# Kernel tuning notes

Measured on AMD Instinct MI355X. Metric: run time of the kernel, lower is better.

## Reference

```python
import jax, jax.numpy as jnp
import numpy as np

EPS = 1e-5
SLOPE = 0.01  # LeakyReLU negative_slope

def _ln(x, g, b):
    m = jnp.mean(x, axis=-1, keepdims=True)
    v = jnp.mean((x - m) ** 2, axis=-1, keepdims=True)
    return (x - m) * jax.lax.rsqrt(v + EPS) * g + b

def _lrelu(x):
    return jnp.where(x >= 0, x, SLOPE * x)

def _s6(x, W1, b1, W2, b2, W3, b3, A):
    # x: (B, L, D); A: (D, N). Mamba-style S6 selective scan.
    Bm = x @ W2 + b2                       # (B, L, N) input-dependent B
    Cm = x @ W3 + b3                       # (B, L, N) input-dependent C
    delta = jax.nn.softplus(x @ W1 + b1)   # (B, L, D) step sizes
    dA = jnp.exp(jnp.einsum('bld,dn->bldn', delta, A))            # (B,L,D,N)
    dBx = jnp.einsum('bld,bln->bldn', delta, Bm) * x[..., None]    # (B,L,D,N) dB * x
    Bsz, L, D = x.shape
    N = A.shape[1]
    def step(h, inp):
        dA_t, dBx_t, C_t = inp
        h = dA_t * h + dBx_t                       # (B, D, N)
        return h, jnp.einsum('bn,bdn->bd', C_t, h)  # y_t: (B, D)
    xs = (jnp.transpose(dA, (1, 0, 2, 3)),
          jnp.transpose(dBx, (1, 0, 2, 3)),
          jnp.transpose(Cm, (1, 0, 2)))
    _, ys = jax.lax.scan(step, jnp.zeros((Bsz, D, N), x.dtype), xs)
    return jnp.transpose(ys, (1, 0, 2))  # (B, L, D)

def _fwd(text, audio, video, tW1, tb1, tg1, tbe1, tW2, tb2, tg2, tbe2, sW1, sb1, sW2, sb2, sW3, sb3, sA, aW1, ab1, ag1, abe1, aW2, ab2, ag2, abe2, vW1, vb1, vg1, vbe1, vW2, vb2, vg2, vbe2, cW1, cb1, cW2, cb2):
    # text branch: Linear+LN+LeakyReLU x2, Dropout(eval=identity), S6
    t = _lrelu(_ln(text @ tW1 + tb1, tg1, tbe1))
    t = _lrelu(_ln(t @ tW2 + tb2, tg2, tbe2))
    t = _s6(t, sW1, sb1, sW2, sb2, sW3, sb3, sA)
    # audio / video branches are computed but do not feed the output (as in source)
    a = _lrelu(_ln(audio @ aW1 + ab1, ag1, abe1))
    a = _lrelu(_ln(a @ aW2 + ab2, ag2, abe2))
    v = _lrelu(_ln(video @ vW1 + vb1, vg1, vbe1))
    v = _lrelu(_ln(v @ vW2 + vb2, vg2, vbe2))
    o1 = t @ cW1 + cb1
    return o1 @ cW2 + cb2  # (B, L, 2)

def setup_inputs() -> dict:
    key = jax.random.key(0)
    ks = iter(jax.random.split(key, 64))
    def W(shape, s=0.05):
        return jax.random.normal(next(ks), shape, jnp.float32) * s
    B, L = 64, 63
    d = {
        'text': jax.random.normal(next(ks), (B, L, 100), jnp.float32),
        'audio': jax.random.normal(next(ks), (B, L, 73), jnp.float32),
        'video': jax.random.normal(next(ks), (B, L, 100), jnp.float32),
        'tW1': W((100, 128)), 'tb1': jnp.zeros(128), 'tg1': jnp.ones(128), 'tbe1': jnp.zeros(128),
        'tW2': W((128, 100)), 'tb2': jnp.zeros(100), 'tg2': jnp.ones(100), 'tbe2': jnp.zeros(100),
        'sW1': W((100, 100)), 'sb1': jnp.zeros(100),
        'sW2': W((100, 300)), 'sb2': jnp.zeros(300),
        'sW3': W((100, 300)), 'sb3': jnp.zeros(300),
        'sA': jnp.full((100, 300), 1.0 / np.sqrt(300.0), jnp.float32),  # F.normalize(ones, dim=-1)
        'aW1': W((73, 256)), 'ab1': jnp.zeros(256), 'ag1': jnp.ones(256), 'abe1': jnp.zeros(256),
        'aW2': W((256, 100)), 'ab2': jnp.zeros(100), 'ag2': jnp.ones(100), 'abe2': jnp.zeros(100),
        'vW1': W((100, 256)), 'vb1': jnp.zeros(256), 'vg1': jnp.ones(256), 'vbe1': jnp.zeros(256),
        'vW2': W((256, 100)), 'vb2': jnp.zeros(100), 'vg2': jnp.ones(100), 'vbe2': jnp.zeros(100),
        'cW1': W((100, 50)), 'cb1': jnp.zeros(50),
        'cW2': W((50, 2)), 'cb2': jnp.zeros(2),
    }
    return d

def reference(text, audio, video, tW1, tb1, tg1, tbe1, tW2, tb2, tg2, tbe2, sW1, sb1, sW2, sb2, sW3, sb3, sA, aW1, ab1, ag1, abe1, aW2, ab2, ag2, abe2, vW1, vb1, vg1, vbe1, vW2, vb2, vg2, vbe2, cW1, cb1, cW2, cb2):
    return _fwd(text, audio, video, tW1, tb1, tg1, tbe1, tW2, tb2, tg2, tbe2, sW1, sb1, sW2, sb2, sW3, sb3, sA, aW1, ab1, ag1, abe1, aW2, ab2, ag2, abe2, vW1, vb1, vg1, vbe1, vW2, vb2, vg2, vbe2, cW1, cb1, cW2, cb2)
```

## Files before the change

### kernel.cpp

```cpp
#include <hip/hip_runtime.h>
#include <hip/hip_bf16.h>


typedef __hip_bfloat16 bf16;

#define BATCH 64
#define SEQ   63
#define ROWS  (BATCH * SEQ)
#define DIN   100
#define H1    128
#define DM    100
#define NS    300

__device__ __forceinline__ float2 up2(unsigned u) {
    float2 r;
    r.x = __uint_as_float(u << 16);
    r.y = __uint_as_float(u & 0xffff0000u);
    return r;
}
template<bool ISB>
__device__ __forceinline__ float LD(const void* p, int i) {
    if (ISB) return __bfloat162float(((const bf16*)p)[i]);
    else     return ((const float*)p)[i];
}
template<bool ISB>
__device__ __forceinline__ float2 LD2(const void* p, int i) {
    if (ISB) return up2(((const unsigned*)p)[i]);
    else     return ((const float2*)p)[i];
}
__device__ __forceinline__ float waveReduceSum(float v) {
#pragma unroll
    for (int off = 32; off > 0; off >>= 1) v += __shfl_xor(v, off, 64);
    return v;
}
__device__ __forceinline__ float4 waveReduceSum4(float4 v) {
#pragma unroll
    for (int off = 32; off > 0; off >>= 1) {
        const float a = __shfl_xor(v.x, off, 64);
        const float b = __shfl_xor(v.y, off, 64);
        const float c = __shfl_xor(v.z, off, 64);
        const float d = __shfl_xor(v.w, off, 64);
        v.x += a; v.y += b; v.z += c; v.w += d;
    }
    return v;
}
__device__ __forceinline__ float lrelu(float x) { return x >= 0.f ? x : 0.01f * x; }
__device__ __forceinline__ float softplusf(float x) {
    return (x > 20.f) ? x : log1pf(__expf(x));
}
__device__ __forceinline__ bool flags_uniform(const float* __restrict__ f) {
    bool u = true;
#pragma unroll
    for (int i = 0; i < 8; ++i) u &= (f[i] > 0.5f);
    return u;
}
__device__ __forceinline__ bool detect_bf16(const unsigned short* __restrict__ probe) {
    const int l = threadIdx.x & 63;
    const unsigned u0 = probe[l * 2];
    const unsigned u1 = probe[l * 2 + 1];
    const float v0 = fabsf(__uint_as_float(u0 << 16));
    const float v1 = fabsf(__uint_as_float(u1 << 16));
    const bool big = !(v0 < 1000.f) || !(v1 < 1000.f);
    const bool zero_even = (u0 == 0u);
    const unsigned long long mb = __ballot(big);
    const unsigned long long mz = __ballot(zero_even);
    return (mb == 0ULL) && (__popcll(mz) < 32);
}

template<bool ISB>
__device__ __forceinline__ void a_main(
    const void* __restrict__ text,
    const void* __restrict__ tW1, const void* __restrict__ tb1,
    const void* __restrict__ tg1, const void* __restrict__ tbe1,
    const void* __restrict__ tW2, const void* __restrict__ tb2,
    const void* __restrict__ tg2, const void* __restrict__ tbe2,
    const void* __restrict__ sW1w, const void* __restrict__ sb1,
    float* __restrict__ ddx, float* __restrict__ t2g,
    float* __restrict__ sW,
    float (&xb)[4][DIN][2], float (&t1b)[4][H1][2], float (&t2b)[4][DM][2])
{
    const int tid  = threadIdx.x;
    const int w    = tid >> 6;
    const int lane = tid & 63;
    const int r0   = blockIdx.x * 8 + w * 2;

    if (lane < 50) {
#pragma unroll
        for (int r = 0; r < 2; ++r) {
            const float2 xv = LD2<ISB>(text, (r0 + r) * 50 + lane);
            xb[w][2 * lane][r]     = xv.x;
            xb[w][2 * lane + 1][r] = xv.y;
        }
    }
    for (int i = tid; i < 6400; i += 256)
        *(float2*)&sW[2 * i] = LD2<ISB>(tW1, i);
    __syncthreads();

    const float2 b1v = LD2<ISB>(tb1, lane);
    float ax0 = b1v.x, ay0 = b1v.y, ax1 = b1v.x, ay1 = b1v.y;
#pragma unroll 10
    for (int k = 0; k < DIN; ++k) {
        const float2 wv = *(const float2*)&sW[k * 128 + 2 * lane];
        const float2 xv = *(const float2*)&xb[w][k][0];
        ax0 += xv.x * wv.x; ay0 += xv.x * wv.y;
        ax1 += xv.y * wv.x; ay1 += xv.y * wv.y;
    }
    {
        float4 red = waveReduceSum4(make_float4(
            ax0 + ay0, ax0 * ax0 + ay0 * ay0,
            ax1 + ay1, ax1 * ax1 + ay1 * ay1));
        const float m0 = red.x * (1.f / 128.f);
        const float rs0 = rsqrtf(red.y * (1.f / 128.f) - m0 * m0 + 1e-5f);
        const float m1 = red.z * (1.f / 128.f);
        const float rs1 = rsqrtf(red.w * (1.f / 128.f) - m1 * m1 + 1e-5f);
        const float2 g = LD2<ISB>(tg1, lane), be = LD2<ISB>(tbe1, lane);
        float2 v;
        v.x = lrelu((ax0 - m0) * rs0 * g.x + be.x);
        v.y = lrelu((ax1 - m1) * rs1 * g.x + be.x);
        *(float2*)&t1b[w][2 * lane][0] = v;
        v.x = lrelu((ay0 - m0) * rs0 * g.y + be.y);
        v.y = lrelu((ay1 - m1) * rs1 * g.y + be.y);
        *(float2*)&t1b[w][2 * lane + 1][0] = v;
    }
    __syncthreads();

    for (int i = tid; i < 6400; i += 256)
        *(float2*)&sW[2 * i] = LD2<ISB>(tW2, i);
    __syncthreads();

    const bool act = lane < 50;
    const int  li  = act ? lane : 0;
    const float2 b2v = LD2<ISB>(tb2, li);
    float cx0 = b2v.x, cy0 = b2v.y, cx1 = b2v.x, cy1 = b2v.y;
#pragma unroll 8
    for (int k = 0; k < H1; ++k) {
        const float2 wv = *(const float2*)&sW[k * 100 + 2 * li];
        const float2 tv = *(const float2*)&t1b[w][k][0];
        cx0 += tv.x * wv.x; cy0 += tv.x * wv.y;
        cx1 += tv.y * wv.x; cy1 += tv.y * wv.y;
    }
    float u0x, u0y, u1x, u1y;
    {
        float4 red = waveReduceSum4(act ? make_float4(
            cx0 + cy0, cx0 * cx0 + cy0 * cy0,
            cx1 + cy1, cx1 * cx1 + cy1 * cy1) : make_float4(0.f, 0.f, 0.f, 0.f));
        const float m0 = red.x * 0.01f;
        const float rs0 = rsqrtf(red.y * 0.01f - m0 * m0 + 1e-5f);
        const float m1 = red.z * 0.01f;
        const float rs1 = rsqrtf(red.w * 0.01f - m1 * m1 + 1e-5f);
        if (act) {
            const float2 g = LD2<ISB>(tg2, lane), be = LD2<ISB>(tbe2, lane);
            u0x = lrelu((cx0 - m0) * rs0 * g.x + be.x);
            u0y = lrelu((cy0 - m0) * rs0 * g.y + be.y);
            u1x = lrelu((cx1 - m1) * rs1 * g.x + be.x);
            u1y = lrelu((cy1 - m1) * rs1 * g.y + be.y);
            t2b[w][2 * lane][0] = u0x; t2b[w][2 * lane + 1][0] = u0y;
            t2b[w][2 * lane][1] = u1x; t2b[w][2 * lane + 1][1] = u1y;
            *(float2*)(t2g + (r0)     * DM + 2 * lane) = make_float2(u0x, u0y);
            *(float2*)(t2g + (r0 + 1) * DM + 2 * lane) = make_float2(u1x, u1y);
        }
    }
    __syncthreads();

    for (int i = tid; i < 5000; i += 256)
        *(float2*)&sW[2 * i] = LD2<ISB>(sW1w, i);
    __syncthreads();

    const float2 sbv = LD2<ISB>(sb1, li);
    float dA0x = sbv.x, dA0y = sbv.y, dA1x = sbv.x, dA1y = sbv.y;
#pragma unroll 10
    for (int k = 0; k < DM; ++k) {
        const float2 wv = *(const float2*)&sW[k * 100 + 2 * li];
        const float2 tv = *(const float2*)&t2b[w][k][0];
        dA0x += tv.x * wv.x; dA0y += tv.x * wv.y;
        dA1x += tv.y * wv.x; dA1y += tv.y * wv.y;
    }
    if (act) {
        float de0 = softplusf(dA0x), de1 = softplusf(dA0y);
        float4 o;
        o.x = de0; o.y = de0 * u0x; o.z = de1; o.w = de1 * u0y;
        *(float4*)(ddx + (r0) * (2 * DM) + 4 * lane) = o;
        de0 = softplusf(dA1x); de1 = softplusf(dA1y);
        o.x = de0; o.y = de0 * u1x; o.z = de1; o.w = de1 * u1y;
        *(float4*)(ddx + (r0 + 1) * (2 * DM) + 4 * lane) = o;
    }
}

template<bool ISB>
__device__ __forceinline__ void a_prep(
    const void* __restrict__ sW2, const void* __restrict__ sb2,
    const void* __restrict__ sW3, const void* __restrict__ sb3,
    float* __restrict__ M33p, float* __restrict__ k0w, float* __restrict__ sW,
    int d3)
{
    const int tid = threadIdx.x;
    const int w = tid >> 6, lane = tid & 63;
    float* W3row = sW;
    float* b2v   = sW + 320;
    float* b3v   = sW + 640;
    for (int i = tid; i < 300; i += 256) {
        W3row[i] = LD<ISB>(sW3, d3 * 300 + i);
        b2v[i]   = LD<ISB>(sb2, i);
        b3v[i]   = LD<ISB>(sb3, i);
    }
    __syncthreads();
    for (int g = 0; g < 6; ++g) {
        const int d2 = w * 25 + g * 4;
        float4 p = make_float4(0.f, 0.f, 0.f, 0.f);
#pragma unroll
        for (int rep = 0; rep < 5; ++rep) {
            const int n = lane + 64 * rep;
            if (n < 300) {
                const float w3 = W3row[n];
                p.x += LD<ISB>(sW2, (d2 + 0) * 300 + n) * w3;
                p.y += LD<ISB>(sW2, (d2 + 1) * 300 + n) * w3;
                p.z += LD<ISB>(sW2, (d2 + 2) * 300 + n) * w3;
                p.w += LD<ISB>(sW2, (d2 + 3) * 300 + n) * w3;
            }
        }
        p = waveReduceSum4(p);
        if (lane == 0) {
            M33p[d3 * 102 + d2 + 0] = p.x;
            M33p[d3 * 102 + d2 + 1] = p.y;
            M33p[d3 * 102 + d2 + 2] = p.z;
            M33p[d3 * 102 + d2 + 3] = p.w;
        }
    }
    {
        const int d2 = w * 25 + 24;
        float4 p = make_float4(0.f, 0.f, 0.f, 0.f);
#pragma unroll
        for (int rep = 0; rep < 5; ++rep) {
            const int n = lane + 64 * rep;
            if (n < 300) {
                p.x += LD<ISB>(sW2, d2 * 300 + n) * W3row[n];
                if (w == 0) p.y += W3row[n] * b2v[n];
                if (w == 1) p.y += LD<ISB>(sW2, d3 * 300 + n) * b3v[n];
                if (w == 2 && d3 == 0) p.y += b2v[n] * b3v[n];
            }
        }
        p = waveReduceSum4(p);
        if (lane == 0) {
            M33p[d3 * 102 + d2] = p.x;
            if (w == 0) M33p[d3 * 102 + 100] = p.y;
            if (w == 1) M33p[d3 * 102 + 101] = p.y;
            if (w == 2 && d3 == 0) k0w[0] = p.y;
        }
    }
}

template<bool ISB>
__device__ __forceinline__ void a_check(
    const void* __restrict__ sA, float* __restrict__ Afl,
    float* __restrict__ sW, int j)
{
    const int tid = threadIdx.x;
    const float a0 = LD<ISB>(sA, 0);
    bool ok = true;
    for (int i = j * 3750 + tid; i < (j + 1) * 3750; i += 256)
        ok &= (LD<ISB>(sA, i) == a0);
    if (tid == 0) sW[960] = 1.f;
    __syncthreads();
    if (!ok) sW[960] = 0.f;
    __syncthreads();
    if (tid == 0) Afl[j] = sW[960];
    if (j == 0 && tid == 1) Afl[8] = a0;
}

template<bool ISB>
__device__ __forceinline__ void a_mkv(
    const void* __restrict__ cW1, const void* __restrict__ cb1,
    const void* __restrict__ cW2, const void* __restrict__ cb2,
    float* __restrict__ Mkv)
{
    const int t = threadIdx.x;
    if (t < 200) {
        const int d = t >> 1, j = t & 1;
        float m = 0.f;
#pragma unroll 5
        for (int i = 0; i < 50; ++i)
            m += LD<ISB>(cW1, d * 50 + i) * LD<ISB>(cW2, 2 * i + j);
        Mkv[t] = m;
    } else if (t < 202) {
        const int j = t - 200;
        float kv = LD<ISB>(cb2, j);
#pragma unroll 5
        for (int i = 0; i < 50; ++i)
            kv += LD<ISB>(cb1, i) * LD<ISB>(cW2, 2 * i + j);
        Mkv[200 + j] = kv;
    }
}

__global__ __launch_bounds__(256) void k_A(
    const void* text,
    const void* tW1, const void* tb1, const void* tg1, const void* tbe1,
    const void* tW2, const void* tb2, const void* tg2, const void* tbe2,
    const void* sW1w, const void* sb1,
    const void* sW2, const void* sb2, const void* sW3, const void* sb3,
    const void* sA,
    const void* cW1, const void* cb1, const void* cW2, const void* cb2,
    float* ddx, float* t2g, float* Mkv, float* M33p, float* k0w, float* Afl,
    const unsigned short* probe)
{
    __shared__ __align__(16) float sW[12800];
    __shared__ __align__(16) float xb[4][DIN][2];
    __shared__ __align__(16) float t1b[4][H1][2];
    __shared__ __align__(16) float t2b[4][DM][2];
    const bool isb = detect_bf16(probe);
    const int blk = blockIdx.x;
    if (blk < 504) {
        if (isb) a_main<true >(text, tW1, tb1, tg1, tbe1, tW2, tb2, tg2, tbe2,
                               sW1w, sb1, ddx, t2g, sW, xb, t1b, t2b);
        else     a_main<false>(text, tW1, tb1, tg1, tbe1, tW2, tb2, tg2, tbe2,
                               sW1w, sb1, ddx, t2g, sW, xb, t1b, t2b);
    } else if (blk < 604) {
        if (isb) a_prep<true >(sW2, sb2, sW3, sb3, M33p, k0w, sW, blk - 504);
        else     a_prep<false>(sW2, sb2, sW3, sb3, M33p, k0w, sW, blk - 504);
    } else if (blk < 612) {
        if (isb) a_check<true >(sA, Afl, sW, blk - 604);
        else     a_check<false>(sA, Afl, sW, blk - 604);
    } else {
        if (isb) a_mkv<true >(cW1, cb1, cW2, cb2, Mkv);
        else     a_mkv<false>(cW1, cb1, cW2, cb2, Mkv);
    }
}

template<bool ISB>
__device__ __forceinline__ void gyh_impl(
    const float* __restrict__ t2g, const float* __restrict__ ddx,
    const float* __restrict__ M33p, const float* __restrict__ k0w,
    const float* __restrict__ Mkv, const float* __restrict__ Afl,
    void* __restrict__ outp,
    float* __restrict__ sBig, float (&sZ)[8][104],
    float* __restrict__ sv, float* __restrict__ srv,
    float (&sG)[8][64], float (&sE)[8][100])
{
    const int bid = blockIdx.x;
    const int xcd = bid & 7;
    const int j   = bid >> 3;
    const int b   = xcd * 8 + (j >> 3);
    const int tc  = j & 7;
    const int tid = threadIdx.x;
    const int w = tid >> 6, lane = tid & 63;

    float* __restrict__ sT2 = sBig;
    float* __restrict__ sV  = sBig;

    for (int i = tid; i < 3150; i += 256) {
        const float2 v = *(const float2*)(t2g + b * 6300 + 2 * i);
        const int t = i / 50, k = 2 * (i % 50);
        sT2[t * 102 + k]     = v.x;
        sT2[t * 102 + k + 1] = v.y;
    }
    if (tid < 100) sv[tid] = M33p[tid * 102 + 101];
    __syncthreads();

    if (lane < 16) {
        const int s = w * 16 + lane;
        if (s < SEQ) {
            float acc = 0.f;
#pragma unroll 4
            for (int k = 0; k < 100; ++k) acc += sT2[s * 102 + k] * sv[k];
            srv[s] = acc;
        }
    }

    {
        const int l2 = (lane < 51) ? 2 * lane : 0;
        int tg2i[2];
#pragma unroll
        for (int r = 0; r < 2; ++r) {
            const int t = tc * 8 + w * 2 + r;
            tg2i[r] = (t < SEQ) ? t : SEQ - 1;
        }
        float2 acc[2];
        acc[0] = make_float2(0.f, 0.f);
        acc[1] = make_float2(0.f, 0.f);
        float2 ring[10];
#pragma unroll
        for (int j2 = 0; j2 < 10; ++j2) ring[j2] = *(const float2*)(M33p + j2 * 102 + l2);
        for (int kk = 0; kk < 100; kk += 10) {
#pragma unroll
            for (int j2 = 0; j2 < 10; ++j2) {
                const int jj = kk + j2;
                const float2 wv = ring[j2];
                if (jj + 10 < 100) ring[j2] = *(const float2*)(M33p + (jj + 10) * 102 + l2);
#pragma unroll
                for (int r = 0; r < 2; ++r) {
                    const float tv = sT2[tg2i[r] * 102 + jj];
                    acc[r].x += tv * wv.x;
                    acc[r].y += tv * wv.y;
                }
            }
        }
        if (lane < 51) {
#pragma unroll
            for (int r = 0; r < 2; ++r)
                *(float2*)&sZ[w * 2 + r][l2] = acc[r];
        }
    }
    __syncthreads();

    {
        const float kz = k0w[0];
        const int s = lane;
        const int sc = (s < SEQ) ? s : SEQ - 1;
        float acc0 = kz + sZ[w * 2][100]     + srv[sc];
        float acc1 = kz + sZ[w * 2 + 1][100] + srv[sc];
#pragma unroll 5
        for (int k2 = 0; k2 < 50; ++k2) {
            const float2 tv = *(const float2*)&sT2[sc * 102 + 2 * k2];
            const float2 z0 = *(const float2*)&sZ[w * 2][2 * k2];
            const float2 z1 = *(const float2*)&sZ[w * 2 + 1][2 * k2];
            acc0 += z0.x * tv.x + z0.y * tv.y;
            acc1 += z1.x * tv.x + z1.y * tv.y;
        }
        if (s < SEQ) {
            if (tc * 8 + w * 2     < SEQ) sG[w * 2][s]     = acc0;
            if (tc * 8 + w * 2 + 1 < SEQ) sG[w * 2 + 1][s] = acc1;
        }
    }
    __syncthreads();

    {
        const float a = Afl[8];
        const int tmax = (tc * 8 + 7 < SEQ) ? tc * 8 + 7 : SEQ - 1;
        if (tid < 100) {
            const int d = tid;
            float D = 0.f;
            for (int s = 0; s <= tmax; ++s) {
                const float2 dn = *(const float2*)(ddx + (b * SEQ + s) * 200 + 2 * d);
                D += dn.x;
                const float E = __expf(a * D);
                sV[d * 65 + s] = dn.y / E;
                const int tl = s - tc * 8;
                if (tl >= 0) sE[tl][d] = E;
            }
        }
    }
    __syncthreads();

    {
        const int li = (lane < 50) ? lane : 49;
        const float4 mk = *(const float4*)(Mkv + 4 * li);
        float4 oacc = make_float4(0.f, 0.f, 0.f, 0.f);
#pragma unroll
        for (int r = 0; r < 2; ++r) {
            const int tl = w * 2 + r;
            const int t  = tc * 8 + tl;
            if (t >= SEQ) continue;
            float acc0 = 0.f, acc1 = 0.f;
            const float* v0 = sV + (2 * li) * 65;
            const float* v1 = sV + (2 * li + 1) * 65;
            for (int s = 0; s <= t; ++s) {
                const float g = sG[tl][s];
                acc0 += g * v0[s];
                acc1 += g * v1[s];
            }
            const float2 E = *(const float2*)&sE[tl][2 * li];
            const float y0 = (lane < 50) ? E.x * acc0 : 0.f;
            const float y1 = (lane < 50) ? E.y * acc1 : 0.f;
            if (r == 0) { oacc.x = y0 * mk.x + y1 * mk.z; oacc.y = y0 * mk.y + y1 * mk.w; }
            else        { oacc.z = y0 * mk.x + y1 * mk.z; oacc.w = y0 * mk.y + y1 * mk.w; }
        }
        oacc = waveReduceSum4(oacc);
        if (lane == 0) {
            const float kv0 = Mkv[200], kv1 = Mkv[201];
#pragma unroll
            for (int r = 0; r < 2; ++r) {
                const int t = tc * 8 + w * 2 + r;
                if (t >= SEQ) continue;
                const int row = b * SEQ + t;
                const float o0 = (r == 0 ? oacc.x : oacc.z) + kv0;
                const float o1 = (r == 0 ? oacc.y : oacc.w) + kv1;
                if (ISB) {
                    ((bf16*)outp)[row * 2 + 0] = __float2bfloat16(o0);
                    ((bf16*)outp)[row * 2 + 1] = __float2bfloat16(o1);
                } else {
                    *(float2*)((float*)outp + row * 2) = make_float2(o0, o1);
                }
            }
        }
    }
}

__global__ __launch_bounds__(256, 4) void k_GYH(
    const float* __restrict__ t2g, const float* __restrict__ ddx,
    const float* __restrict__ M33p, const float* __restrict__ k0w,
    const float* __restrict__ Mkv, const float* __restrict__ Afl,
    void* __restrict__ outp, const unsigned short* __restrict__ probe)
{
    __shared__ __align__(16) float sBig[64 * 102];
    __shared__ __align__(16) float sZ[8][104];
    __shared__ float sv[100];
    __shared__ float srv[64];
    __shared__ __align__(16) float sG[8][64];
    __shared__ __align__(16) float sE[8][100];
    if (!flags_uniform(Afl)) return;
    if (detect_bf16(probe))
        gyh_impl<true >(t2g, ddx, M33p, k0w, Mkv, Afl, outp, sBig, sZ, sv, srv, sG, sE);
    else
        gyh_impl<false>(t2g, ddx, M33p, k0w, Mkv, Afl, outp, sBig, sZ, sv, srv, sG, sE);
}

template<bool ISB>
__device__ __forceinline__ float4 LD4(const void* p, int i) {
    if (ISB) {
        const uint2 u = ((const uint2*)p)[i];
        float4 r;
        r.x = __uint_as_float(u.x << 16);
        r.y = __uint_as_float(u.x & 0xffff0000u);
        r.z = __uint_as_float(u.y << 16);
        r.w = __uint_as_float(u.y & 0xffff0000u);
        return r;
    } else return ((const float4*)p)[i];
}

template<bool ISB>
__device__ __forceinline__ void b_impl(
    const float* __restrict__ t2g,
    const void* __restrict__ sW2, const void* __restrict__ sb2,
    const void* __restrict__ sW3, const void* __restrict__ sb3,
    float* __restrict__ BC, float (&sT)[DM][8])
{
    const int t  = threadIdx.x;
    const int r0 = blockIdx.x * 8;
    if (t < DM) {
#pragma unroll
        for (int r = 0; r < 8; ++r) sT[t][r] = t2g[(r0 + r) * DM + t];
    }
    __syncthreads();
    const bool isB = t < 75;
    const bool valid = t < 150;
    const int colbase = isB ? 4 * t : (valid ? 4 * (t - 75) : 0);
    const void* Wp   = isB ? sW2 : sW3;
    const void* bias = isB ? sb2 : sb3;
    const int rs4 = NS >> 2;
    const int cb4 = colbase >> 2;
    float4 acc[8];
    {
        const float4 bv = LD4<ISB>(bias, cb4);
#pragma unroll
        for (int r = 0; r < 8; ++r) acc[r] = bv;
    }
    float4 ring[4];
#pragma unroll
    for (int j = 0; j < 4; ++j) ring[j] = LD4<ISB>(Wp, j * rs4 + cb4);
    for (int kk = 0; kk < DM; kk += 4) {
#pragma unroll
        for (int j = 0; j < 4; ++j) {
            const int k = kk + j;
            const float4 wv = ring[j];
            if (k + 4 < DM) ring[j] = LD4<ISB>(Wp, (k + 4) * rs4 + cb4);
            const float4 lo = *(const float4*)&sT[k][0];
            const float4 hi = *(const float4*)&sT[k][4];
            acc[0].x += lo.x * wv.x; acc[0].y += lo.x * wv.y; acc[0].z += lo.x * wv.z; acc[0].w += lo.x * wv.w;
            acc[1].x += lo.y * wv.x; acc[1].y += lo.y * wv.y; acc[1].z += lo.y * wv.z; acc[1].w += lo.y * wv.w;
            acc[2].x += lo.z * wv.x; acc[2].y += lo.z * wv.y; acc[2].z += lo.z * wv.z; acc[2].w += lo.z * wv.w;
            acc[3].x += lo.w * wv.x; acc[3].y += lo.w * wv.y; acc[3].z += lo.w * wv.z; acc[3].w += lo.w * wv.w;
            acc[4].x += hi.x * wv.x; acc[4].y += hi.x * wv.y; acc[4].z += hi.x * wv.z; acc[4].w += hi.x * wv.w;
            acc[5].x += hi.y * wv.x; acc[5].y += hi.y * wv.y; acc[5].z += hi.y * wv.z; acc[5].w += hi.y * wv.w;
            acc[6].x += hi.z * wv.x; acc[6].y += hi.z * wv.y; acc[6].z += hi.z * wv.z; acc[6].w += hi.z * wv.w;
            acc[7].x += hi.w * wv.x; acc[7].y += hi.w * wv.y; acc[7].z += hi.w * wv.z; acc[7].w += hi.w * wv.w;
        }
    }
    if (valid) {
        const int off = isB ? 0 : 1;
#pragma unroll
        for (int r = 0; r < 8; ++r) {
            float* bp = BC + (r0 + r) * (2 * NS) + 2 * colbase + off;
            bp[0] = acc[r].x; bp[2] = acc[r].y;
            bp[4] = acc[r].z; bp[6] = acc[r].w;
        }
    }
}

__global__ __launch_bounds__(192, 1) void k_B(
    const float* t2g, const void* sW2, const void* sb2,
    const void* sW3, const void* sb3, float* BC,
    const float* Afl, const unsigned short* probe)
{
    __shared__ __align__(16) float sT[DM][8];
    if (flags_uniform(Afl)) return;
    if (detect_bf16(probe)) b_impl<true >(t2g, sW2, sb2, sW3, sb3, BC, sT);
    else                    b_impl<false>(t2g, sW2, sb2, sW3, sb3, BC, sT);
}

template<bool ISB>
__device__ __forceinline__ void scan_impl(
    const float* __restrict__ ddx, const float* __restrict__ BC,
    const void* __restrict__ sA, float* __restrict__ y,
    float (&sacc)[4][16][2][68])
{
    const int w    = threadIdx.x >> 6;
    const int lane = threadIdx.x & 63;
    const int wid  = blockIdx.x * 4 + w;
    const int b    = wid / 50;
    const int dp   = wid % 50;
    const int d0   = 2 * dp, d1 = d0 + 1;

    int nc[5]; bool nv[5];
    float A0[5], A1[5], h0[5], h1[5];
#pragma unroll
    for (int c = 0; c < 5; ++c) {
        const int n = lane + 64 * c;
        nv[c] = n < NS;
        nc[c] = nv[c] ? n : 0;
        A0[c] = nv[c] ? LD<ISB>(sA, d0 * NS + nc[c]) : 0.f;
        A1[c] = nv[c] ? LD<ISB>(sA, d1 * NS + nc[c]) : 0.f;
        h0[c] = 0.f; h1[c] = 0.f;
    }
    const float* ddp = ddx + (b * SEQ) * (2 * DM) + 4 * dp;
    const float* BCp = BC  + (b * SEQ) * (2 * NS);
    float*       yp  = y   + (b * SEQ) * DM + d0;

    float4 pdd[3];
    float2 pbc[3][5];
#pragma unroll
    for (int j = 0; j < 3; ++j) {
        pdd[j] = *(const float4*)(ddp + j * (2 * DM));
#pragma unroll
        for (int c = 0; c < 5; ++c)
            pbc[j][c] = nv[c] ? *(const float2*)(BCp + j * (2 * NS) + 2 * nc[c])
                              : make_float2(0.f, 0.f);
    }
    const int pr = lane >> 1;
    const int hh = lane & 1;
    const int sa = pr & 15;
    const int aa = pr >> 4;

#pragma unroll 3
    for (int l = 0; l < SEQ; ++l) {
        const int bi = l % 3;
        const float4 dd = pdd[bi];
        float2 bc[5];
#pragma unroll
        for (int c = 0; c < 5; ++c) bc[c] = pbc[bi][c];
        if (l + 3 < SEQ) {
            pdd[bi] = *(const float4*)(ddp + (l + 3) * (2 * DM));
#pragma unroll
            for (int c = 0; c < 5; ++c)
                pbc[bi][c] = nv[c] ? *(const float2*)(BCp + (l + 3) * (2 * NS) + 2 * nc[c])
                                   : make_float2(0.f, 0.f);
        }
        float a0 = 0.f, a1 = 0.f;
#pragma unroll
        for (int c = 0; c < 5; ++c) {
            h0[c] = __expf(dd.x * A0[c]) * h0[c] + dd.y * bc[c].x;
            a0 += bc[c].y * h0[c];
            h1[c] = __expf(dd.z * A1[c]) * h1[c] + dd.w * bc[c].x;
            a1 += bc[c].y * h1[c];
        }
        const int s = l & 15;
        sacc[w][s][0][lane] = a0;
        sacc[w][s][1][lane] = a1;

        if (s == 15 || l == SEQ - 1) {
            const int l0 = l & ~15;
            const int cs = l - l0 + 1;
            float sum = 0.f;
            if (sa < cs) {
                const float* rowp = &sacc[w][sa][aa][hh * 32];
#pragma unroll
                for (int i = 0; i < 8; ++i) {
                    const float4 v = *(const float4*)(rowp + 4 * i);
                    sum += v.x + v.y + v.z + v.w;
                }
            }
            sum += __shfl_xor(sum, 1, 64);
            if (hh == 0 && sa < cs) yp[(l0 + sa) * DM + aa] = sum;
        }
    }
}

__global__ __launch_bounds__(256) void k_scan(
    const float* ddx, const float* BC, const void* sA, float* y,
    const float* Afl, const unsigned short* probe)
{
    __shared__ __align__(16) float sacc[4][16][2][68];
    if (flags_uniform(Afl)) return;
    if (detect_bf16(probe)) scan_impl<true >(ddx, BC, sA, y, sacc);
    else                    scan_impl<false>(ddx, BC, sA, y, sacc);
}

template<bool ISB>
__device__ __forceinline__ void headf_impl(
    const float* __restrict__ y, const float* __restrict__ Mkv,
    void* __restrict__ outp)
{
    const int row = blockIdx.x * 256 + threadIdx.x;
    if (row >= ROWS) return;
    float a0 = Mkv[200], a1 = Mkv[201];
    const float* yr = y + row * DM;
#pragma unroll 4
    for (int k = 0; k < DM; ++k) {
        const float v = yr[k];
        const float2 m = *(const float2*)(Mkv + 2 * k);
        a0 += v * m.x;
        a1 += v * m.y;
    }
    if (ISB) {
        ((bf16*)outp)[row * 2 + 0] = __float2bfloat16(a0);
        ((bf16*)outp)[row * 2 + 1] = __float2bfloat16(a1);
    } else {
        *(float2*)((float*)outp + row * 2) = make_float2(a0, a1);
    }
}

__global__ __launch_bounds__(256) void k_headF(
    const float* y, const float* Mkv, void* outp,
    const float* Afl, const unsigned short* probe)
{
    if (flags_uniform(Afl)) return;
    if (detect_bf16(probe)) headf_impl<true >(y, Mkv, outp);
    else                    headf_impl<false>(y, Mkv, outp);
}

extern "C" void kernel_launch(void* const* d_in, const int* in_sizes, int n_in,
                              void* d_out, int out_size, void* d_ws, size_t ws_size,
                              hipStream_t stream)
{
    const void* text = d_in[0];
    const void* tW1  = d_in[3];
    const void* tb1  = d_in[4];
    const void* tg1  = d_in[5];
    const void* tbe1 = d_in[6];
    const void* tW2  = d_in[7];
    const void* tb2  = d_in[8];
    const void* tg2  = d_in[9];
    const void* tbe2 = d_in[10];
    const void* sW1  = d_in[11];
    const void* sb1  = d_in[12];
    const void* sW2  = d_in[13];
    const void* sb2  = d_in[14];
    const void* sW3  = d_in[15];
    const void* sb3  = d_in[16];
    const void* sA   = d_in[17];
    const void* cW1  = d_in[34];
    const void* cb1  = d_in[35];
    const void* cW2  = d_in[36];
    const void* cb2  = d_in[37];
    const unsigned short* probe = (const unsigned short*)d_in[3];

    float* ws   = (float*)d_ws;
    float* ddx  = ws;
    float* BCv  = ddx + ROWS * 2 * DM;
    float* yv   = BCv + ROWS * 2 * NS;
    float* Mkv  = yv + ROWS * DM;
    float* M33p = Mkv + 202;
    float* k0w  = M33p + 10200;
    float* Afl  = k0w + 1;
    float* t2g  = yv;

    k_A<<<613, 256, 0, stream>>>(
        text, tW1, tb1, tg1, tbe1, tW2, tb2, tg2, tbe2,
        sW1, sb1, sW2, sb2, sW3, sb3, sA,
        cW1, cb1, cW2, cb2,
        ddx, t2g, Mkv, M33p, k0w, Afl, probe);

    k_GYH<<<BATCH * 8, 256, 0, stream>>>(t2g, ddx, M33p, k0w, Mkv, Afl,
                                         d_out, probe);

    k_B<<<ROWS / 8, 192, 0, stream>>>(t2g, sW2, sb2, sW3, sb3, BCv, Afl, probe);
    k_scan<<<3200 / 4, 256, 0, stream>>>(ddx, BCv, sA, yv, Afl, probe);
    k_headF<<<(ROWS + 255) / 256, 256, 0, stream>>>(yv, Mkv, d_out, Afl, probe);
}
```

Before: 192.6 us.

## Restructure GYH kernel into 512-thread blocks of 16 timesteps with LDS-staged weights

Each k_GYH block now handles 16 timesteps per batch with 512 threads, halving the block count. The M33p weights, Mkv and the ddx rows are staged into shared memory instead of being read repeatedly from global memory, and the srv dot product becomes a wave reduction. The causal accumulation is unrolled in pairs and the decay factors are precomputed into LDS. This cuts redundant global traffic and per-block setup, at the cost of much higher LDS use per block (about 78 KB), which lowers occupancy.

Result: faster. 179.2 us (-7.0%).

```diff
diff --git a/kernel.cpp b/kernel.cpp
--- a/kernel.cpp
+++ b/kernel.cpp
@@ -331,110 +331,118 @@
     const float* __restrict__ M33p, const float* __restrict__ k0w,
     const float* __restrict__ Mkv, const float* __restrict__ Afl,
     void* __restrict__ outp,
-    float* __restrict__ sBig, float (&sZ)[8][104],
-    float* __restrict__ sv, float* __restrict__ srv,
-    float (&sG)[8][64], float (&sE)[8][100])
+    float* __restrict__ sT2, float* __restrict__ sM,
+    float* __restrict__ sZ, float* __restrict__ sG,
+    float* __restrict__ srv, float* __restrict__ sMk)
 {
     const int bid = blockIdx.x;
     const int xcd = bid & 7;
-    const int j   = bid >> 3;
-    const int b   = xcd * 8 + (j >> 3);
-    const int tc  = j & 7;
+    const int jj  = bid >> 3;
+    const int b   = xcd * 8 + (jj >> 2);
+    const int q   = jj & 3;
     const int tid = threadIdx.x;
     const int w = tid >> 6, lane = tid & 63;
 
-    float* __restrict__ sT2 = sBig;
-    float* __restrict__ sV  = sBig;
-
-    for (int i = tid; i < 3150; i += 256) {
-        const float2 v = *(const float2*)(t2g + b * 6300 + 2 * i);
-        const int t = i / 50, k = 2 * (i % 50);
-        sT2[t * 102 + k]     = v.x;
-        sT2[t * 102 + k + 1] = v.y;
-    }
-    if (tid < 100) sv[tid] = M33p[tid * 102 + 101];
-    __syncthreads();
-
-    if (lane < 16) {
-        const int s = w * 16 + lane;
-        if (s < SEQ) {
-            float acc = 0.f;
+    const int tmax  = (q * 16 + 15 < SEQ) ? q * 16 + 15 : SEQ - 1;
+    const int srows = tmax + 1;
+
+    for (int i = tid; i < srows * 50; i += 512) {
+        const float2 v = ((const float2*)t2g)[b * 3150 + i];
+        const int t = i / 50, k2 = i % 50;
+        sT2[t * 102 + 2 * k2]     = v.x;
+        sT2[t * 102 + 2 * k2 + 1] = v.y;
+    }
+    for (int i = tid; i < 5100; i += 512)
+        *(float2*)&sM[2 * i] = ((const float2*)M33p)[i];
+    if (tid < 202) sMk[tid] = Mkv[tid];
+    __syncthreads();
+
+    {
+        const float mv0 = sM[lane * 102 + 101];
+        const float mv1 = (lane < 36) ? sM[(64 + lane) * 102 + 101] : 0.f;
+#pragma unroll
+        for (int g = 0; g < 2; ++g) {
+            float4 p;
+            float acc[4];
+#pragma unroll
+            for (int i = 0; i < 4; ++i) {
+                const int s = w * 8 + g * 4 + i;
+                const int scl = (s <= tmax) ? s : 0;
+                float a = sT2[scl * 102 + lane] * mv0;
+                if (lane < 36) a += sT2[scl * 102 + 64 + lane] * mv1;
+                acc[i] = a;
+            }
+            p = waveReduceSum4(make_float4(acc[0], acc[1], acc[2], acc[3]));
+            if (lane == 0) {
+                const int s0 = w * 8 + g * 4;
+                srv[s0 + 0] = p.x; srv[s0 + 1] = p.y;
+                srv[s0 + 2] = p.z; srv[s0 + 3] = p.w;
+            }
+        }
+    }
+    {
+        const int l2 = (lane < 51) ? 2 * lane : 0;
+        const int zr0 = w * 2, zr1 = w * 2 + 1;
+        const int t0 = q * 16 + zr0;
+        const int t1 = q * 16 + zr1;
+        const int tc1 = (t1 <= tmax) ? t1 : tmax;
+        float2 a0 = make_float2(0.f, 0.f);
+        float2 a1 = make_float2(0.f, 0.f);
 #pragma unroll 4
-            for (int k = 0; k < 100; ++k) acc += sT2[s * 102 + k] * sv[k];
-            srv[s] = acc;
-        }
-    }
-
-    {
-        const int l2 = (lane < 51) ? 2 * lane : 0;
-        int tg2i[2];
-#pragma unroll
-        for (int r = 0; r < 2; ++r) {
-            const int t = tc * 8 + w * 2 + r;
-            tg2i[r] = (t < SEQ) ? t : SEQ - 1;
-        }
-        float2 acc[2];
-        acc[0] = make_float2(0.f, 0.f);
-        acc[1] = make_float2(0.f, 0.f);
-        float2 ring[10];
-#pragma unroll
-        for (int j2 = 0; j2 < 10; ++j2) ring[j2] = *(const float2*)(M33p + j2 * 102 + l2);
-        for (int kk = 0; kk < 100; kk += 10) {
-#pragma unroll
-            for (int j2 = 0; j2 < 10; ++j2) {
-                const int jj = kk + j2;
-                const float2 wv = ring[j2];
-                if (jj + 10 < 100) ring[j2] = *(const float2*)(M33p + (jj + 10) * 102 + l2);
-#pragma unroll
-                for (int r = 0; r < 2; ++r) {
-                    const float tv = sT2[tg2i[r] * 102 + jj];
-                    acc[r].x += tv * wv.x;
-                    acc[r].y += tv * wv.y;
-                }
-            }
+        for (int k = 0; k < 100; ++k) {
+            const float2 wv = *(const float2*)&sM[k * 102 + l2];
+            const float x0 = sT2[t0 * 102 + k];
+            const float x1 = sT2[tc1 * 102 + k];
+            a0.x += x0 * wv.x; a0.y += x0 * wv.y;
+            a1.x += x1 * wv.x; a1.y += x1 * wv.y;
         }
         if (lane < 51) {
-#pragma unroll
-            for (int r = 0; r < 2; ++r)
-                *(float2*)&sZ[w * 2 + r][l2] = acc[r];
+            *(float2*)&sZ[zr0 * 102 + l2] = a0;
+            if (t1 <= tmax) *(float2*)&sZ[zr1 * 102 + l2] = a1;
         }
     }
     __syncthreads();
 
     {
         const float kz = k0w[0];
-        const int s = lane;
-        const int sc = (s < SEQ) ? s : SEQ - 1;
-        float acc0 = kz + sZ[w * 2][100]     + srv[sc];
-        float acc1 = kz + sZ[w * 2 + 1][100] + srv[sc];
+        const int sc  = (lane <= tmax) ? lane : tmax;
+        const int zr0 = w * 2, zr1 = w * 2 + 1;
+        const int t1  = q * 16 + zr1;
+        float g0 = kz + sZ[zr0 * 102 + 100] + srv[sc];
+        float g1 = kz + sZ[zr1 * 102 + 100] + srv[sc];
 #pragma unroll 5
         for (int k2 = 0; k2 < 50; ++k2) {
             const float2 tv = *(const float2*)&sT2[sc * 102 + 2 * k2];
-            const float2 z0 = *(const float2*)&sZ[w * 2][2 * k2];
-            const float2 z1 = *(const float2*)&sZ[w * 2 + 1][2 * k2];
-            acc0 += z0.x * tv.x + z0.y * tv.y;
-            acc1 += z1.x * tv.x + z1.y * tv.y;
-        }
-        if (s < SEQ) {
-            if (tc * 8 + w * 2     < SEQ) sG[w * 2][s]     = acc0;
-            if (tc * 8 + w * 2 + 1 < SEQ) sG[w * 2 + 1][s] = acc1;
-        }
-    }
-    __syncthreads();
-
-    {
-        const float a = Afl[8];
-        const int tmax = (tc * 8 + 7 < SEQ) ? tc * 8 + 7 : SEQ - 1;
+            const float2 z0 = *(const float2*)&sZ[zr0 * 102 + 2 * k2];
+            const float2 z1 = *(const float2*)&sZ[zr1 * 102 + 2 * k2];
+            g0 += z0.x * tv.x + z0.y * tv.y;
+            g1 += z1.x * tv.x + z1.y * tv.y;
+        }
+        if (lane <= tmax) {
+            sG[zr0 * 64 + lane] = g0;
+            if (t1 <= tmax) sG[zr1 * 64 + lane] = g1;
+        }
+    }
+    __syncthreads();
+
+    for (int i = tid; i < srows * 100; i += 512) {
+        const float2 v = ((const float2*)ddx)[b * 6300 + i];
+        sT2[i] = v.x;
+        sM[i]  = v.y;
+    }
+    __syncthreads();
+
+    {
+        const float av = Afl[8];
         if (tid < 100) {
             const int d = tid;
             float D = 0.f;
             for (int s = 0; s <= tmax; ++s) {
-                const float2 dn = *(const float2*)(ddx + (b * SEQ + s) * 200 + 2 * d);
-                D += dn.x;
-                const float E = __expf(a * D);
-                sV[d * 65 + s] = dn.y / E;
-                const int tl = s - tc * 8;
-                if (tl >= 0) sE[tl][d] = E;
+                D += sT2[s * 100 + d];
+                const float En = __expf(-av * D);
+                sM[s * 100 + d] = sM[s * 100 + d] * En;
+                const int zr = s - q * 16;
+                if (zr >= 0) sM[6400 + zr * 100 + d] = __expf(av * D);
             }
         }
     }
@@ -442,37 +450,48 @@
 
     {
         const int li = (lane < 50) ? lane : 49;
-        const float4 mk = *(const float4*)(Mkv + 4 * li);
-        float4 oacc = make_float4(0.f, 0.f, 0.f, 0.f);
+        const float4 mk = *(const float4*)&sMk[4 * li];
+        float4 oc = make_float4(0.f, 0.f, 0.f, 0.f);
 #pragma unroll
         for (int r = 0; r < 2; ++r) {
-            const int tl = w * 2 + r;
-            const int t  = tc * 8 + tl;
-            if (t >= SEQ) continue;
-            float acc0 = 0.f, acc1 = 0.f;
-            const float* v0 = sV + (2 * li) * 65;
-            const float* v1 = sV + (2 * li + 1) * 65;
-            for (int s = 0; s <= t; ++s) {
-                const float g = sG[tl][s];
-                acc0 += g * v0[s];
-                acc1 += g * v1[s];
+            const int zr = w * 2 + r;
+            const int t  = q * 16 + zr;
+            float o0 = 0.f, o1 = 0.f;
+            if (t < SEQ) {
+                float a0 = 0.f, a1 = 0.f;
+                const int nf = (t + 1) >> 1;
+                const float* gp = &sG[zr * 64];
+                for (int s2 = 0; s2 < nf; ++s2) {
+                    const float2 g2 = *(const float2*)&gp[2 * s2];
+                    const float2 v0 = *(const float2*)&sM[(2 * s2) * 100 + 2 * li];
+                    const float2 v1 = *(const float2*)&sM[(2 * s2 + 1) * 100 + 2 * li];
+                    a0 += g2.x * v0.x + g2.y * v1.x;
+                    a1 += g2.x * v0.y + g2.y * v1.y;
+                }
+                if ((t & 1) == 0) {
+                    const float gg = gp[t];
+                    const float2 vt = *(const float2*)&sM[t * 100 + 2 * li];
+                    a0 += gg * vt.x; a1 += gg * vt.y;
+                }
+                const float2 e2 = *(const float2*)&sM[6400 + zr * 100 + 2 * li];
+                const float y0 = (lane < 50) ? e2.x * a0 : 0.f;
+                const float y1 = (lane < 50) ? e2.y * a1 : 0.f;
+                o0 = y0 * mk.x + y1 * mk.z;
+                o1 = y0 * mk.y + y1 * mk.w;
             }
-            const float2 E = *(const float2*)&sE[tl][2 * li];
-            const float y0 = (lane < 50) ? E.x * acc0 : 0.f;
-            const float y1 = (lane < 50) ? E.y * acc1 : 0.f;
-            if (r == 0) { oacc.x = y0 * mk.x + y1 * mk.z; oacc.y = y0 * mk.y + y1 * mk.w; }
-            else        { oacc.z = y0 * mk.x + y1 * mk.z; oacc.w = y0 * mk.y + y1 * mk.w; }
-        }
-        oacc = waveReduceSum4(oacc);
+            if (r == 0) { oc.x = o0; oc.y = o1; }
+            else        { oc.z = o0; oc.w = o1; }
+        }
+        oc = waveReduceSum4(oc);
         if (lane == 0) {
-            const float kv0 = Mkv[200], kv1 = Mkv[201];
+            const float kv0 = sMk[200], kv1 = sMk[201];
 #pragma unroll
             for (int r = 0; r < 2; ++r) {
-                const int t = tc * 8 + w * 2 + r;
+                const int t = q * 16 + w * 2 + r;
                 if (t >= SEQ) continue;
                 const int row = b * SEQ + t;
-                const float o0 = (r == 0 ? oacc.x : oacc.z) + kv0;
-                const float o1 = (r == 0 ? oacc.y : oacc.w) + kv1;
+                const float o0 = (r == 0 ? oc.x : oc.z) + kv0;
+                const float o1 = (r == 0 ? oc.y : oc.w) + kv1;
                 if (ISB) {
                     ((bf16*)outp)[row * 2 + 0] = __float2bfloat16(o0);
                     ((bf16*)outp)[row * 2 + 1] = __float2bfloat16(o1);
@@ -484,23 +503,23 @@
     }
 }
 
-__global__ __launch_bounds__(256, 4) void k_GYH(
+__global__ __launch_bounds__(512) void k_GYH(
     const float* __restrict__ t2g, const float* __restrict__ ddx,
     const float* __restrict__ M33p, const float* __restrict__ k0w,
     const float* __restrict__ Mkv, const float* __restrict__ Afl,
     void* __restrict__ outp, const unsigned short* __restrict__ probe)
 {
-    __shared__ __align__(16) float sBig[64 * 102];
-    __shared__ __align__(16) float sZ[8][104];
-    __shared__ float sv[100];
-    __shared__ float srv[64];
-    __shared__ __align__(16) float sG[8][64];
-    __shared__ __align__(16) float sE[8][100];
+    __shared__ __align__(16) float sT2[6426];
+    __shared__ __align__(16) float sM[10240];
+    __shared__ __align__(16) float sZ[1632];
+    __shared__ __align__(16) float sG[1024];
+    __shared__ __align__(16) float srv[64];
+    __shared__ __align__(16) float sMk[204];
     if (!flags_uniform(Afl)) return;
     if (detect_bf16(probe))
-        gyh_impl<true >(t2g, ddx, M33p, k0w, Mkv, Afl, outp, sBig, sZ, sv, srv, sG, sE);
+        gyh_impl<true >(t2g, ddx, M33p, k0w, Mkv, Afl, outp, sT2, sM, sZ, sG, srv, sMk);
     else
-        gyh_impl<false>(t2g, ddx, M33p, k0w, Mkv, Afl, outp, sBig, sZ, sv, srv, sG, sE);
+        gyh_impl<false>(t2g, ddx, M33p, k0w, Mkv, Afl, outp, sT2, sM, sZ, sG, srv, sMk);
 }
 
 template<bool ISB>
@@ -758,7 +777,7 @@
         cW1, cb1, cW2, cb2,
         ddx, t2g, Mkv, M33p, k0w, Afl, probe);
 
-    k_GYH<<<BATCH * 8, 256, 0, stream>>>(t2g, ddx, M33p, k0w, Mkv, Afl,
+    k_GYH<<<BATCH * 4, 512, 0, stream>>>(t2g, ddx, M33p, k0w, Mkv, Afl,
                                          d_out, probe);
 
     k_B<<<ROWS / 8, 192, 0, stream>>>(t2g, sW2, sb2, sW3, sb3, BCv, Afl, probe);
```
